# Optimization experiments

Measured on AMD Instinct MI355X. Metric: run time of the kernel, lower is better.

## Reference

```python
import jax, jax.numpy as jnp
import numpy as np

B, NB, BS, F = 4, 16, 256, 1024   # batch, num_blocks, block_size, features
H, D = 16, 64                     # heads, head_dim
ROPE = 32                         # rope_rotary_dims


def rotate_every_two(x):
    x1 = x[..., ::2]
    x2 = x[..., 1::2]
    return jnp.stack([-x2, x1], axis=-1).reshape(x.shape)


def apply_rope(x, num_blocks, block_size):
    # x: [B, NB, BS, H, rope_dim]
    rope_dim = x.shape[-1]
    inv_freq = 1.0 / 10000.0 ** (jnp.arange(0, rope_dim, 2, dtype=jnp.float32) / rope_dim)
    pos = jnp.arange(num_blocks * block_size, dtype=jnp.float32)
    ang = pos[:, None] * inv_freq[None, :]                       # [S, rope_dim/2]
    sin = jnp.sin(ang).reshape(num_blocks, block_size, rope_dim // 2)
    cos = jnp.cos(ang).reshape(num_blocks, block_size, rope_dim // 2)
    sin = jnp.repeat(sin[None, :, :, None, :], 2, axis=-1)       # [1, NB, BS, 1, rope_dim]
    cos = jnp.repeat(cos[None, :, :, None, :], 2, axis=-1)
    return x * cos + rotate_every_two(x) * sin


def setup_inputs() -> dict:
    key = jax.random.key(0)
    ks = jax.random.split(key, 8)
    s_in = 1.0 / np.sqrt(F)
    s_out = 1.0 / np.sqrt(H * D)
    return {
        "inputs_q": jax.random.normal(ks[0], (B, NB, BS, F), jnp.float32),
        "inputs_kv": jax.random.normal(ks[1], (B, NB, BS, F), jnp.float32),
        "Wq": jax.random.normal(ks[2], (F, H, D), jnp.float32) * s_in,
        "bq": jnp.zeros((H, D), jnp.float32),
        "Wk": jax.random.normal(ks[3], (F, H, D), jnp.float32) * s_in,
        "bk": jnp.zeros((H, D), jnp.float32),
        "Wv": jax.random.normal(ks[4], (F, H, D), jnp.float32) * s_in,
        "bv": jnp.zeros((H, D), jnp.float32),
        "Wo": jax.random.normal(ks[5], (H, D, F), jnp.float32) * s_out,
        "bo": jnp.zeros((F,), jnp.float32),
    }


def reference(inputs_q, inputs_kv, Wq, bq, Wk, bk, Wv, bv, Wo, bo):
    # QKV projections: [B, NB, BS, F] x [F, H, D] -> [B, NB, BS, H, D]
    q = jnp.einsum("bnsf,fhd->bnshd", inputs_q, Wq) + bq
    k = jnp.einsum("bnsf,fhd->bnshd", inputs_kv, Wk) + bk
    v = jnp.einsum("bnsf,fhd->bnshd", inputs_kv, Wv) + bv

    # RoPE on first ROPE dims of head_dim (intended semantics per docstring)
    q_rot, q_pass = q[..., :ROPE], q[..., ROPE:]
    k_rot, k_pass = k[..., :ROPE], k[..., ROPE:]
    q = jnp.concatenate([apply_rope(q_rot, NB, BS), q_pass], axis=-1)
    k = jnp.concatenate([apply_rope(k_rot, NB, BS), k_pass], axis=-1)

    # block-local dot-product attention (flax nn.dot_product_attention semantics)
    q = q / jnp.sqrt(jnp.asarray(D, q.dtype))
    scores = jnp.einsum("bnqhd,bnkhd->bnhqk", q, k)              # [B, NB, H, BS, BS]
    weights = jax.nn.softmax(scores, axis=-1)
    x = jnp.einsum("bnhqk,bnkhd->bnqhd", weights, v)             # [B, NB, BS, H, D]

    # output projection over (heads, head_dim)
    out = jnp.einsum("bnqhd,hdf->bnqf", x, Wo) + bo              # [B, NB, BS, F]
    return out
```

## Files before the change

kernel.cpp:

```cpp
#include <hip/hip_runtime.h>

typedef __attribute__((ext_vector_type(4))) float f32x4;
typedef __attribute__((ext_vector_type(8))) short s16x8;
typedef __attribute__((ext_vector_type(4))) unsigned short u16x4;

struct F2 { float c, s; };

__device__ __forceinline__ unsigned short f2b(float f) {
  unsigned u = __builtin_bit_cast(unsigned, f);
  u += 0x7FFFu + ((u >> 16) & 1u);
  return (unsigned short)(u >> 16);
}
__device__ __forceinline__ void gll16(const void* g, void* l) {
  __builtin_amdgcn_global_load_lds(
      (const __attribute__((address_space(1))) unsigned int*)g,
      (__attribute__((address_space(3))) unsigned int*)l, 16, 0, 0);
}
__device__ __forceinline__ f32x4 mfma16(s16x8 a, s16x8 b, f32x4 c) {
  return __builtin_amdgcn_mfma_f32_16x16x32_bf16(a, b, c, 0, 0, 0);
}

__global__ void k_cvt(const float* __restrict__ src, unsigned short* __restrict__ dst, int n4) {
  int i = blockIdx.x * 256 + threadIdx.x;
  int stride = gridDim.x * 256;
  for (; i < n4; i += stride) {
    f32x4 v = ((const f32x4*)src)[i];
    u16x4 o;
    o.x = f2b(v.x); o.y = f2b(v.y); o.z = f2b(v.z); o.w = f2b(v.w);
    ((u16x4*)dst)[i] = o;
  }
}

__global__ void k_sincos(F2* __restrict__ tab) {
  int idx = blockIdx.x * 256 + threadIdx.x;
  int pos = idx >> 4, fi = idx & 15;
  double inv = exp((double)fi * (-9.210340371976184 / 16.0));
  double a = (double)pos * inv;
  F2 r; r.c = (float)cos(a); r.s = (float)sin(a);
  tab[idx] = r;
}

__global__ void k_transpose(const float* __restrict__ wq,
                            const float* __restrict__ wk,
                            const float* __restrict__ wv,
                            const float* __restrict__ wo,
                            unsigned short* __restrict__ wtqkv,
                            unsigned short* __restrict__ wto) {
  __shared__ unsigned short tile[32][33];
  int z = blockIdx.z;
  const float* src = (z == 0) ? wq : (z == 1) ? wk : (z == 2) ? wv : wo;
  unsigned short* dst = (z < 3) ? (wtqkv + (size_t)z * 1048576) : wto;
  int bx = blockIdx.x * 32, by = blockIdx.y * 32;
  tile[threadIdx.y][threadIdx.x] = f2b(src[(size_t)(by + threadIdx.y) * 1024 + bx + threadIdx.x]);
  __syncthreads();
  dst[(size_t)(bx + threadIdx.y) * 1024 + by + threadIdx.x] = tile[threadIdx.x][threadIdx.y];
}

__device__ __forceinline__ void gemm_core(
    const unsigned short* __restrict__ Ag, const unsigned short* __restrict__ Bg,
    int m0, int n0, unsigned short* Sh, f32x4 (&acc)[8][4]) {
  const int tid = threadIdx.x, wid = tid >> 6, lane = tid & 63;
  const int fr = lane & 15, fg = lane >> 4, f7 = fr & 7;
  const int wm = wid >> 2, wn = wid & 3;
  const int rowoff = lane >> 3;
  const int lanecol = ((lane & 7) ^ rowoff) * 8;
  const int g0 = (fg ^ f7) * 8, g1 = ((4 + fg) ^ f7) * 8;

  auto SA = [&](int T, int ah) {
    unsigned short* dstb = Sh + (T & 1) * 32768;
#pragma unroll
    for (int i = 0; i < 2; ++i) {
      int rloc = ah * 128 + (wid * 2 + i) * 8;
      gll16(Ag + (size_t)(m0 + rloc + rowoff) * 1024 + T * 64 + lanecol, dstb + rloc * 64);
    }
  };
  auto SB = [&](int T, int bh) {
    unsigned short* dstb = Sh + (T & 1) * 32768 + 16384;
#pragma unroll
    for (int i = 0; i < 2; ++i) {
      int rloc = bh * 128 + (wid * 2 + i) * 8;
      gll16(Bg + (size_t)(n0 + rloc + rowoff) * 1024 + T * 64 + lanecol, dstb + rloc * 64);
    }
  };

  SA(0, 0); SA(0, 1); SB(0, 0); SB(0, 1); SA(1, 0); SA(1, 1);
  asm volatile("s_waitcnt vmcnt(4)" ::: "memory");
  __builtin_amdgcn_sched_barrier(0);
  __builtin_amdgcn_s_barrier();

  for (int t = 0; t < 16; ++t) {
    const unsigned short* bufA = Sh + (t & 1) * 32768;
    const unsigned short* bufB = bufA + 16384;
    s16x8 a0[4][2], a1[4][2], b0[2][2], b1[2][2];
#pragma unroll
    for (int mf = 0; mf < 4; ++mf) {
      const unsigned short* r = &bufA[(wm * 128 + mf * 16 + fr) * 64];
      a0[mf][0] = *(const s16x8*)&r[g0];
      a0[mf][1] = *(const s16x8*)&r[g1];
    }
#pragma unroll
    for (int nf = 0; nf < 2; ++nf) {
      const unsigned short* r = &bufB[(wn * 64 + nf * 16 + fr) * 64];
      b0[nf][0] = *(const s16x8*)&r[g0];
      b0[nf][1] = *(const s16x8*)&r[g1];
    }
    if (t + 1 < 16) SB(t + 1, 0);
    __builtin_amdgcn_s_barrier();
    asm volatile("s_waitcnt lgkmcnt(0)" ::: "memory");
    __builtin_amdgcn_sched_barrier(0);
    __builtin_amdgcn_s_setprio(1);
#pragma unroll
    for (int mf = 0; mf < 4; ++mf)
#pragma unroll
      for (int nf = 0; nf < 2; ++nf) {
        acc[mf][nf] = mfma16(a0[mf][0], b0[nf][0], acc[mf][nf]);
        acc[mf][nf] = mfma16(a0[mf][1], b0[nf][1], acc[mf][nf]);
      }
    __builtin_amdgcn_s_setprio(0);
    __builtin_amdgcn_s_barrier();
#pragma unroll
    for (int mf = 0; mf < 4; ++mf) {
      const unsigned short* r = &bufA[(wm * 128 + 64 + mf * 16 + fr) * 64];
      a1[mf][0] = *(const s16x8*)&r[g0];
      a1[mf][1] = *(const s16x8*)&r[g1];
    }
    if (t + 1 < 16) SB(t + 1, 1);
    __builtin_amdgcn_s_barrier();
    asm volatile("s_waitcnt lgkmcnt(0)" ::: "memory");
    __builtin_amdgcn_sched_barrier(0);
    __builtin_amdgcn_s_setprio(1);
#pragma unroll
    for (int mf = 0; mf < 4; ++mf)
#pragma unroll
      for (int nf = 0; nf < 2; ++nf) {
        acc[4 + mf][nf] = mfma16(a1[mf][0], b0[nf][0], acc[4 + mf][nf]);
        acc[4 + mf][nf] = mfma16(a1[mf][1], b0[nf][1], acc[4 + mf][nf]);
      }
    __builtin_amdgcn_s_setprio(0);
    __builtin_amdgcn_s_barrier();
#pragma unroll
    for (int nf = 0; nf < 2; ++nf) {
      const unsigned short* r = &bufB[(wn * 64 + 32 + nf * 16 + fr) * 64];
      b1[nf][0] = *(const s16x8*)&r[g0];
      b1[nf][1] = *(const s16x8*)&r[g1];
    }
    if (t + 2 < 16) SA(t + 2, 0);
    __builtin_amdgcn_s_barrier();
    asm volatile("s_waitcnt lgkmcnt(0)" ::: "memory");
    __builtin_amdgcn_sched_barrier(0);
    __builtin_amdgcn_s_setprio(1);
#pragma unroll
    for (int mf = 0; mf < 4; ++mf)
#pragma unroll
      for (int nf = 0; nf < 2; ++nf) {
        acc[4 + mf][2 + nf] = mfma16(a1[mf][0], b1[nf][0], acc[4 + mf][2 + nf]);
        acc[4 + mf][2 + nf] = mfma16(a1[mf][1], b1[nf][1], acc[4 + mf][2 + nf]);
      }
    __builtin_amdgcn_s_setprio(0);
    __builtin_amdgcn_s_barrier();
    if (t + 2 < 16) SA(t + 2, 1);
    if (t < 14) asm volatile("s_waitcnt vmcnt(4)" ::: "memory");
    else        asm volatile("s_waitcnt vmcnt(0)" ::: "memory");
    __builtin_amdgcn_sched_barrier(0);
    __builtin_amdgcn_s_barrier();
    __builtin_amdgcn_s_setprio(1);
#pragma unroll
    for (int mf = 0; mf < 4; ++mf)
#pragma unroll
      for (int nf = 0; nf < 2; ++nf) {
        acc[mf][2 + nf] = mfma16(a0[mf][0], b1[nf][0], acc[mf][2 + nf]);
        acc[mf][2 + nf] = mfma16(a0[mf][1], b1[nf][1], acc[mf][2 + nf]);
      }
    __builtin_amdgcn_s_setprio(0);
    __builtin_amdgcn_s_barrier();
  }
}

__global__ __launch_bounds__(512, 1) void k_qkv(
    const unsigned short* __restrict__ Xq,
    const unsigned short* __restrict__ Xkv,
    const unsigned short* __restrict__ WT,
    const float* __restrict__ bq,
    const float* __restrict__ bk,
    const float* __restrict__ bv,
    const F2* __restrict__ tab,
    unsigned short* __restrict__ qbuf,
    unsigned short* __restrict__ kbuf,
    unsigned short* __restrict__ vbuf) {
  __shared__ __align__(16) unsigned short S[65536];
  int bid = blockIdx.x;
  int swz = (bid & 7) * 96 + (bid >> 3);
  int mt = swz / 12, nt = swz % 12;
  int m0 = mt * 256, n0 = nt * 256;
  int which = n0 >> 10;
  const unsigned short* X = (which == 0) ? Xq : Xkv;
  const float* bias = (which == 0) ? bq : (which == 1) ? bk : bv;
  unsigned short* dst = (which == 0) ? qbuf : (which == 1) ? kbuf : vbuf;
  int n0l = n0 & 1023;
  int tid = threadIdx.x, wid = tid >> 6, lane = tid & 63;
  int fr = lane & 15, fg = lane >> 4;
  int wm = wid >> 2, wn = wid & 3;

  f32x4 acc[8][4] = {};
  gemm_core(X, WT, m0, n0, S, acc);

  unsigned short* W = S + wid * 8192;
  int hh = (n0l + wn * 64) >> 6;
  int bn = m0 >> 8;
#pragma unroll
  for (int nf = 0; nf < 4; ++nf) {
    int d = nf * 16 + fr;
    int col = n0l + wn * 64 + d;
    float bz = bias[col];
    bool rope = (which < 2) && (nf < 2);
#pragma unroll
    for (int mf = 0; mf < 8; ++mf) {
#pragma unroll
      for (int j = 0; j < 4; ++j) {
        int row = mf * 16 + fg * 4 + j;
        int mg = m0 + wm * 128 + row;
        float v = acc[mf][nf][j] + bz;
        if (rope) {
          float p = __shfl_xor(v, 1);
          F2 cs = tab[(mg & 4095) * 16 + (d >> 1)];
          v = (d & 1) ? fmaf(v, cs.c, p * cs.s) : fmaf(v, cs.c, -(p * cs.s));
        }
        if (which == 0) v *= 0.125f;
        W[row * 64 + (((d >> 3) ^ (row & 7)) << 3) + (d & 7)] = f2b(v);
      }
    }
  }
  asm volatile("s_waitcnt lgkmcnt(0)" ::: "memory");
  __builtin_amdgcn_sched_barrier(0);
  size_t gbase = ((size_t)(bn * 16 + hh) * 256 + wm * 128) * 64;
#pragma unroll
  for (int it = 0; it < 16; ++it) {
    int r = it * 8 + (lane >> 3);
    int ch = (lane & 7) ^ (r & 7);
    s16x8 vv = *(const s16x8*)&W[r * 64 + ch * 8];
    *(s16x8*)&dst[gbase + r * 64 + (lane & 7) * 8] = vv;
  }
}

__global__ __launch_bounds__(512, 1) void k_attn(
    const unsigned short* __restrict__ qbuf,
    const unsigned short* __restrict__ kbuf,
    const unsigned short* __restrict__ vbuf,
    unsigned short* __restrict__ xbuf) {
  __shared__ __align__(16) unsigned short Kl[256 * 64];
  __shared__ __align__(16) unsigned short Vt[64 * 264];
  __shared__ __align__(16) unsigned short Pl[8][16 * 264];
  int gb = blockIdx.x;
  size_t base = (size_t)gb * (256 * 64);
  const unsigned short* Q = qbuf + base;
  const unsigned short* K = kbuf + base;
  const unsigned short* V = vbuf + base;
  int bn = gb >> 4, h = gb & 15;
  int tid = threadIdx.x, wid = tid >> 6, lane = tid & 63;
  int fr = lane & 15, fg = lane >> 4;

#pragma unroll
  for (int tt = 0; tt < 4; ++tt) {
    int t = wid * 4 + tt;
    int r = t * 8 + (lane >> 3);
    int csrc = (lane & 7) ^ (r & 7);
    gll16(K + r * 64 + csrc * 8, &Kl[t * 512]);
  }
  {
    int rv = tid >> 1, chalf = (tid & 1) * 32;
#pragma unroll
    for (int c8 = 0; c8 < 4; ++c8) {
      s16x8 vv = *(const s16x8*)&V[rv * 64 + chalf + c8 * 8];
#pragma unroll
      for (int j = 0; j < 8; ++j)
        Vt[(chalf + c8 * 8 + j) * 264 + rv] = (unsigned short)vv[j];
    }
  }
  __syncthreads();

  unsigned short* P = Pl[wid];
  int f7 = fr & 7;
  int c0 = (fg ^ f7) * 8;
  int c1 = ((4 + fg) ^ f7) * 8;
  for (int mtile = 0; mtile < 2; ++mtile) {
    int q0 = wid * 32 + mtile * 16;
    s16x8 qa0 = *(const s16x8*)&Q[(q0 + fr) * 64 + fg * 8];
    s16x8 qa1 = *(const s16x8*)&Q[(q0 + fr) * 64 + 32 + fg * 8];
    f32x4 sc[16] = {};
#pragma unroll
    for (int nt = 0; nt < 16; ++nt) {
      int rr = nt * 16 + fr;
      s16x8 kb0 = *(const s16x8*)&Kl[rr * 64 + c0];
      sc[nt] = mfma16(qa0, kb0, sc[nt]);
      s16x8 kb1 = *(const s16x8*)&Kl[rr * 64 + c1];
      sc[nt] = mfma16(qa1, kb1, sc[nt]);
    }
    float rs[4];
#pragma unroll
    for (int j = 0; j < 4; ++j) {
      float m = sc[0][j];
#pragma unroll
      for (int nt = 1; nt < 16; ++nt) m = fmaxf(m, sc[nt][j]);
      m = fmaxf(m, __shfl_xor(m, 1));
      m = fmaxf(m, __shfl_xor(m, 2));
      m = fmaxf(m, __shfl_xor(m, 4));
      m = fmaxf(m, __shfl_xor(m, 8));
      float sum = 0.f;
#pragma unroll
      for (int nt = 0; nt < 16; ++nt) {
        float p = __expf(sc[nt][j] - m);
        sum += p;
        P[(fg * 4 + j) * 264 + nt * 16 + fr] = f2b(p);
      }
      sum += __shfl_xor(sum, 1);
      sum += __shfl_xor(sum, 2);
      sum += __shfl_xor(sum, 4);
      sum += __shfl_xor(sum, 8);
      rs[j] = 1.0f / sum;
    }
    f32x4 o[4] = {};
#pragma unroll
    for (int ks = 0; ks < 8; ++ks) {
      s16x8 pa = *(const s16x8*)&P[fr * 264 + ks * 32 + fg * 8];
#pragma unroll
      for (int nt = 0; nt < 4; ++nt) {
        s16x8 vb = *(const s16x8*)&Vt[(nt * 16 + fr) * 264 + ks * 32 + fg * 8];
        o[nt] = mfma16(pa, vb, o[nt]);
      }
    }
#pragma unroll
    for (int nt = 0; nt < 4; ++nt)
#pragma unroll
      for (int j = 0; j < 4; ++j) {
        int srow = q0 + fg * 4 + j;
        int d = nt * 16 + fr;
        xbuf[((size_t)(bn * 256 + srow)) * 1024 + h * 64 + d] = f2b(o[nt][j] * rs[j]);
      }
  }
}

__global__ __launch_bounds__(512, 1) void k_out(
    const unsigned short* __restrict__ Xb,
    const unsigned short* __restrict__ WT,
    const float* __restrict__ bo,
    float* __restrict__ out) {
  __shared__ __align__(16) unsigned short S[65536];
  int bid = blockIdx.x;
  int swz = (bid & 7) * 32 + (bid >> 3);
  int mt = swz >> 2, nt = swz & 3;
  int m0 = mt * 256, n0 = nt * 256;
  int tid = threadIdx.x, wid = tid >> 6, lane = tid & 63;
  int fr = lane & 15, fg = lane >> 4;
  int wm = wid >> 2, wn = wid & 3;

  f32x4 acc[8][4] = {};
  gemm_core(Xb, WT, m0, n0, S, acc);

  float* Wf = (float*)S + wid * 4096;
#pragma unroll
  for (int p = 0; p < 2; ++p) {
#pragma unroll
    for (int nf = 0; nf < 4; ++nf) {
      int d = nf * 16 + fr;
      float bz = bo[n0 + wn * 64 + d];
#pragma unroll
      for (int mf = 0; mf < 4; ++mf) {
#pragma unroll
        for (int j = 0; j < 4; ++j) {
          int row = mf * 16 + fg * 4 + j;
          Wf[row * 64 + d] = acc[p * 4 + mf][nf][j] + bz;
        }
      }
    }
    asm volatile("s_waitcnt lgkmcnt(0)" ::: "memory");
    __builtin_amdgcn_sched_barrier(0);
#pragma unroll
    for (int it = 0; it < 16; ++it) {
      int r = it * 4 + (lane >> 4);
      f32x4 vv = *(const f32x4*)&Wf[r * 64 + (lane & 15) * 4];
      int mg = m0 + wm * 128 + p * 64 + r;
      *(f32x4*)&out[(size_t)mg * 1024 + n0 + wn * 64 + (lane & 15) * 4] = vv;
    }
    asm volatile("s_waitcnt lgkmcnt(0)" ::: "memory");
    __builtin_amdgcn_sched_barrier(0);
  }
}

extern "C" void kernel_launch(void* const* d_in, const int* in_sizes, int n_in,
                              void* d_out, int out_size, void* d_ws, size_t ws_size,
                              hipStream_t stream) {
  const float* Xq  = (const float*)d_in[0];
  const float* Xkv = (const float*)d_in[1];
  const float* Wq  = (const float*)d_in[2];
  const float* bq  = (const float*)d_in[3];
  const float* Wk  = (const float*)d_in[4];
  const float* bk  = (const float*)d_in[5];
  const float* Wv  = (const float*)d_in[6];
  const float* bv  = (const float*)d_in[7];
  const float* Wo  = (const float*)d_in[8];
  const float* bo  = (const float*)d_in[9];
  float* out = (float*)d_out;

  char* ws = (char*)d_ws;
  size_t off = 0;
  F2* tab = (F2*)(ws + off);                           off += (size_t)65536 * sizeof(F2);
  unsigned short* WTqkv = (unsigned short*)(ws + off); off += (size_t)3 * 1048576 * 2;
  unsigned short* WTo   = (unsigned short*)(ws + off); off += (size_t)1048576 * 2;
  unsigned short* Xqb   = (unsigned short*)(ws + off); off += (size_t)16777216 * 2;
  unsigned short* Xkvb  = (unsigned short*)(ws + off); off += (size_t)16777216 * 2;
  unsigned short* qb = (unsigned short*)(ws + off); off += (size_t)16777216 * 2;
  unsigned short* kb = (unsigned short*)(ws + off); off += (size_t)16777216 * 2;
  unsigned short* vb = (unsigned short*)(ws + off); off += (size_t)16777216 * 2;
  unsigned short* xb = Xqb;

  k_cvt<<<2048, 256, 0, stream>>>(Xq,  Xqb,  4194304);
  k_cvt<<<2048, 256, 0, stream>>>(Xkv, Xkvb, 4194304);
  k_sincos<<<256, 256, 0, stream>>>(tab);
  k_transpose<<<dim3(32, 32, 4), dim3(32, 32), 0, stream>>>(Wq, Wk, Wv, Wo, WTqkv, WTo);
  k_qkv<<<768, 512, 0, stream>>>(Xqb, Xkvb, WTqkv, bq, bk, bv, tab, qb, kb, vb);
  k_attn<<<1024, 512, 0, stream>>>(qb, kb, vb, xb);
  k_out<<<256, 512, 0, stream>>>(xb, WTo, bo, out);
}
```

Measured before the change: 283.8 us.

## Switch GEMM core to 32x32x16 bf16 MFMA with reordered A/B prefetch

Replaces the 16x16x32 MFMA tiles in the shared GEMM core with 32x32x16 bf16 MFMAs, restructuring per-wave fragments into 2x2 blocks of 32x32 accumulators. The LDS fragment loads and prefetch order change so A is streamed one stage ahead and B two stages ahead, and the QKV and output epilogues are remapped to the 32x32 accumulator layout. The aim is fewer MFMA issues and fewer LDS reads per FLOP. In exchange the register footprint and LDS access pattern change, and the swizzle now has to stay bank-conflict free for 32-row reads.

```diff
diff --git a/kernel.cpp b/kernel.cpp
--- a/kernel.cpp
+++ b/kernel.cpp
@@ -1,6 +1,7 @@
 #include <hip/hip_runtime.h>
 
 typedef __attribute__((ext_vector_type(4))) float f32x4;
+typedef __attribute__((ext_vector_type(16))) float f32x16;
 typedef __attribute__((ext_vector_type(8))) short s16x8;
 typedef __attribute__((ext_vector_type(4))) unsigned short u16x4;
 
@@ -18,6 +19,9 @@
 }
 __device__ __forceinline__ f32x4 mfma16(s16x8 a, s16x8 b, f32x4 c) {
   return __builtin_amdgcn_mfma_f32_16x16x32_bf16(a, b, c, 0, 0, 0);
+}
+__device__ __forceinline__ f32x16 mfma32(s16x8 a, s16x8 b, f32x16 c) {
+  return __builtin_amdgcn_mfma_f32_32x32x16_bf16(a, b, c, 0, 0, 0);
 }
 
 __global__ void k_cvt(const float* __restrict__ src, unsigned short* __restrict__ dst, int n4) {
@@ -58,13 +62,15 @@
 
 __device__ __forceinline__ void gemm_core(
     const unsigned short* __restrict__ Ag, const unsigned short* __restrict__ Bg,
-    int m0, int n0, unsigned short* Sh, f32x4 (&acc)[8][4]) {
+    int m0, int n0, unsigned short* Sh, f32x16 (&acc)[4][2]) {
   const int tid = threadIdx.x, wid = tid >> 6, lane = tid & 63;
-  const int fr = lane & 15, fg = lane >> 4, f7 = fr & 7;
+  const int l31 = lane & 31, l5 = lane >> 5, r7 = lane & 7;
   const int wm = wid >> 2, wn = wid & 3;
   const int rowoff = lane >> 3;
   const int lanecol = ((lane & 7) ^ rowoff) * 8;
-  const int g0 = (fg ^ f7) * 8, g1 = ((4 + fg) ^ f7) * 8;
+  int gk[4];
+#pragma unroll
+  for (int ks = 0; ks < 4; ++ks) gk[ks] = ((ks * 2 + l5) ^ r7) * 8;
 
   auto SA = [&](int T, int ah) {
     unsigned short* dstb = Sh + (T & 1) * 32768;
@@ -83,7 +89,7 @@
     }
   };
 
-  SA(0, 0); SA(0, 1); SB(0, 0); SB(0, 1); SA(1, 0); SA(1, 1);
+  SA(0, 0); SA(0, 1); SB(0, 0); SB(0, 1); SB(1, 0); SB(1, 1);
   asm volatile("s_waitcnt vmcnt(4)" ::: "memory");
   __builtin_amdgcn_sched_barrier(0);
   __builtin_amdgcn_s_barrier();
@@ -91,86 +97,70 @@
   for (int t = 0; t < 16; ++t) {
     const unsigned short* bufA = Sh + (t & 1) * 32768;
     const unsigned short* bufB = bufA + 16384;
-    s16x8 a0[4][2], a1[4][2], b0[2][2], b1[2][2];
-#pragma unroll
-    for (int mf = 0; mf < 4; ++mf) {
-      const unsigned short* r = &bufA[(wm * 128 + mf * 16 + fr) * 64];
-      a0[mf][0] = *(const s16x8*)&r[g0];
-      a0[mf][1] = *(const s16x8*)&r[g1];
-    }
-#pragma unroll
-    for (int nf = 0; nf < 2; ++nf) {
-      const unsigned short* r = &bufB[(wn * 64 + nf * 16 + fr) * 64];
-      b0[nf][0] = *(const s16x8*)&r[g0];
-      b0[nf][1] = *(const s16x8*)&r[g1];
-    }
-    if (t + 1 < 16) SB(t + 1, 0);
+    s16x8 alo[2][4], ahi[2][4], b0[4], b1[4];
+#pragma unroll
+    for (int mb = 0; mb < 2; ++mb)
+#pragma unroll
+      for (int ks = 0; ks < 4; ++ks)
+        alo[mb][ks] = *(const s16x8*)&bufA[(wm * 128 + mb * 32 + l31) * 64 + gk[ks]];
+#pragma unroll
+    for (int ks = 0; ks < 4; ++ks)
+      b0[ks] = *(const s16x8*)&bufB[(wn * 64 + l31) * 64 + gk[ks]];
+    if (t + 1 < 16) SA(t + 1, 0);
     __builtin_amdgcn_s_barrier();
     asm volatile("s_waitcnt lgkmcnt(0)" ::: "memory");
     __builtin_amdgcn_sched_barrier(0);
     __builtin_amdgcn_s_setprio(1);
 #pragma unroll
-    for (int mf = 0; mf < 4; ++mf)
-#pragma unroll
-      for (int nf = 0; nf < 2; ++nf) {
-        acc[mf][nf] = mfma16(a0[mf][0], b0[nf][0], acc[mf][nf]);
-        acc[mf][nf] = mfma16(a0[mf][1], b0[nf][1], acc[mf][nf]);
-      }
+    for (int ks = 0; ks < 4; ++ks)
+#pragma unroll
+      for (int mb = 0; mb < 2; ++mb)
+        acc[mb][0] = mfma32(alo[mb][ks], b0[ks], acc[mb][0]);
     __builtin_amdgcn_s_setprio(0);
     __builtin_amdgcn_s_barrier();
 #pragma unroll
-    for (int mf = 0; mf < 4; ++mf) {
-      const unsigned short* r = &bufA[(wm * 128 + 64 + mf * 16 + fr) * 64];
-      a1[mf][0] = *(const s16x8*)&r[g0];
-      a1[mf][1] = *(const s16x8*)&r[g1];
-    }
-    if (t + 1 < 16) SB(t + 1, 1);
+    for (int ks = 0; ks < 4; ++ks)
+      b1[ks] = *(const s16x8*)&bufB[(wn * 64 + 32 + l31) * 64 + gk[ks]];
+    if (t + 1 < 16) SA(t + 1, 1);
     __builtin_amdgcn_s_barrier();
     asm volatile("s_waitcnt lgkmcnt(0)" ::: "memory");
     __builtin_amdgcn_sched_barrier(0);
     __builtin_amdgcn_s_setprio(1);
 #pragma unroll
-    for (int mf = 0; mf < 4; ++mf)
-#pragma unroll
-      for (int nf = 0; nf < 2; ++nf) {
-        acc[4 + mf][nf] = mfma16(a1[mf][0], b0[nf][0], acc[4 + mf][nf]);
-        acc[4 + mf][nf] = mfma16(a1[mf][1], b0[nf][1], acc[4 + mf][nf]);
-      }
+    for (int ks = 0; ks < 4; ++ks)
+#pragma unroll
+      for (int mb = 0; mb < 2; ++mb)
+        acc[mb][1] = mfma32(alo[mb][ks], b1[ks], acc[mb][1]);
     __builtin_amdgcn_s_setprio(0);
     __builtin_amdgcn_s_barrier();
 #pragma unroll
-    for (int nf = 0; nf < 2; ++nf) {
-      const unsigned short* r = &bufB[(wn * 64 + 32 + nf * 16 + fr) * 64];
-      b1[nf][0] = *(const s16x8*)&r[g0];
-      b1[nf][1] = *(const s16x8*)&r[g1];
-    }
-    if (t + 2 < 16) SA(t + 2, 0);
+    for (int mb = 0; mb < 2; ++mb)
+#pragma unroll
+      for (int ks = 0; ks < 4; ++ks)
+        ahi[mb][ks] = *(const s16x8*)&bufA[(wm * 128 + 64 + mb * 32 + l31) * 64 + gk[ks]];
+    if (t + 2 < 16) SB(t + 2, 0);
     __builtin_amdgcn_s_barrier();
     asm volatile("s_waitcnt lgkmcnt(0)" ::: "memory");
     __builtin_amdgcn_sched_barrier(0);
     __builtin_amdgcn_s_setprio(1);
 #pragma unroll
-    for (int mf = 0; mf < 4; ++mf)
-#pragma unroll
-      for (int nf = 0; nf < 2; ++nf) {
-        acc[4 + mf][2 + nf] = mfma16(a1[mf][0], b1[nf][0], acc[4 + mf][2 + nf]);
-        acc[4 + mf][2 + nf] = mfma16(a1[mf][1], b1[nf][1], acc[4 + mf][2 + nf]);
-      }
+    for (int ks = 0; ks < 4; ++ks)
+#pragma unroll
+      for (int mb = 0; mb < 2; ++mb)
+        acc[2 + mb][0] = mfma32(ahi[mb][ks], b0[ks], acc[2 + mb][0]);
     __builtin_amdgcn_s_setprio(0);
     __builtin_amdgcn_s_barrier();
-    if (t + 2 < 16) SA(t + 2, 1);
+    if (t + 2 < 16) SB(t + 2, 1);
     if (t < 14) asm volatile("s_waitcnt vmcnt(4)" ::: "memory");
     else        asm volatile("s_waitcnt vmcnt(0)" ::: "memory");
     __builtin_amdgcn_sched_barrier(0);
     __builtin_amdgcn_s_barrier();
     __builtin_amdgcn_s_setprio(1);
 #pragma unroll
-    for (int mf = 0; mf < 4; ++mf)
-#pragma unroll
-      for (int nf = 0; nf < 2; ++nf) {
-        acc[mf][2 + nf] = mfma16(a0[mf][0], b1[nf][0], acc[mf][2 + nf]);
-        acc[mf][2 + nf] = mfma16(a0[mf][1], b1[nf][1], acc[mf][2 + nf]);
-      }
+    for (int ks = 0; ks < 4; ++ks)
+#pragma unroll
+      for (int mb = 0; mb < 2; ++mb)
+        acc[2 + mb][1] = mfma32(ahi[mb][ks], b1[ks], acc[2 + mb][1]);
     __builtin_amdgcn_s_setprio(0);
     __builtin_amdgcn_s_barrier();
   }
@@ -198,28 +188,28 @@
   unsigned short* dst = (which == 0) ? qbuf : (which == 1) ? kbuf : vbuf;
   int n0l = n0 & 1023;
   int tid = threadIdx.x, wid = tid >> 6, lane = tid & 63;
-  int fr = lane & 15, fg = lane >> 4;
+  int l31 = lane & 31, l5 = lane >> 5;
   int wm = wid >> 2, wn = wid & 3;
 
-  f32x4 acc[8][4] = {};
+  f32x16 acc[4][2] = {};
   gemm_core(X, WT, m0, n0, S, acc);
 
   unsigned short* W = S + wid * 8192;
   int hh = (n0l + wn * 64) >> 6;
   int bn = m0 >> 8;
 #pragma unroll
-  for (int nf = 0; nf < 4; ++nf) {
-    int d = nf * 16 + fr;
+  for (int nb = 0; nb < 2; ++nb) {
+    int d = nb * 32 + l31;
     int col = n0l + wn * 64 + d;
     float bz = bias[col];
-    bool rope = (which < 2) && (nf < 2);
-#pragma unroll
-    for (int mf = 0; mf < 8; ++mf) {
-#pragma unroll
-      for (int j = 0; j < 4; ++j) {
-        int row = mf * 16 + fg * 4 + j;
+    bool rope = (which < 2) && (nb == 0);
+#pragma unroll
+    for (int mbi = 0; mbi < 4; ++mbi) {
+#pragma unroll
+      for (int r = 0; r < 16; ++r) {
+        int row = mbi * 32 + (r & 3) + 8 * (r >> 2) + 4 * l5;
         int mg = m0 + wm * 128 + row;
-        float v = acc[mf][nf][j] + bz;
+        float v = acc[mbi][nb][r] + bz;
         if (rope) {
           float p = __shfl_xor(v, 1);
           F2 cs = tab[(mg & 4095) * 16 + (d >> 1)];
@@ -350,25 +340,25 @@
   int mt = swz >> 2, nt = swz & 3;
   int m0 = mt * 256, n0 = nt * 256;
   int tid = threadIdx.x, wid = tid >> 6, lane = tid & 63;
-  int fr = lane & 15, fg = lane >> 4;
+  int l31 = lane & 31, l5 = lane >> 5;
   int wm = wid >> 2, wn = wid & 3;
 
-  f32x4 acc[8][4] = {};
+  f32x16 acc[4][2] = {};
   gemm_core(Xb, WT, m0, n0, S, acc);
 
   float* Wf = (float*)S + wid * 4096;
 #pragma unroll
   for (int p = 0; p < 2; ++p) {
 #pragma unroll
-    for (int nf = 0; nf < 4; ++nf) {
-      int d = nf * 16 + fr;
+    for (int nb = 0; nb < 2; ++nb) {
+      int d = nb * 32 + l31;
       float bz = bo[n0 + wn * 64 + d];
 #pragma unroll
-      for (int mf = 0; mf < 4; ++mf) {
-#pragma unroll
-        for (int j = 0; j < 4; ++j) {
-          int row = mf * 16 + fg * 4 + j;
-          Wf[row * 64 + d] = acc[p * 4 + mf][nf][j] + bz;
+      for (int mbh = 0; mbh < 2; ++mbh) {
+#pragma unroll
+        for (int r = 0; r < 16; ++r) {
+          int row = mbh * 32 + (r & 3) + 8 * (r >> 2) + 4 * l5;
+          Wf[row * 64 + d] = acc[p * 2 + mbh][nb][r] + bz;
         }
       }
     }
```

New measurement: 307.3 us. +8.3%, slower.

## Fuse fp32-to-bf16 input conversion into QKV GEMM A-tile loading

Applied to the files above, without the earlier changes.

Removes the separate k_cvt passes over both fp32 activation tensors. The QKV GEMM now reads fp32 A tiles through registers, converts them to bf16, and writes them into swizzled LDS, with a reworked pipeline that interleaves these loads and writes between MFMA phases. This saves a full write and re-read of 64 MB of bf16 intermediates. In exchange the GEMM reads twice the A bytes per tile, uses more registers, and no longer gets asynchronous direct-to-LDS loads for A, so it may stall more.

```diff
diff --git a/kernel.cpp b/kernel.cpp
--- a/kernel.cpp
+++ b/kernel.cpp
@@ -18,17 +18,6 @@
 }
 __device__ __forceinline__ f32x4 mfma16(s16x8 a, s16x8 b, f32x4 c) {
   return __builtin_amdgcn_mfma_f32_16x16x32_bf16(a, b, c, 0, 0, 0);
-}
-
-__global__ void k_cvt(const float* __restrict__ src, unsigned short* __restrict__ dst, int n4) {
-  int i = blockIdx.x * 256 + threadIdx.x;
-  int stride = gridDim.x * 256;
-  for (; i < n4; i += stride) {
-    f32x4 v = ((const f32x4*)src)[i];
-    u16x4 o;
-    o.x = f2b(v.x); o.y = f2b(v.y); o.z = f2b(v.z); o.w = f2b(v.w);
-    ((u16x4*)dst)[i] = o;
-  }
 }
 
 __global__ void k_sincos(F2* __restrict__ tab) {
@@ -56,7 +45,7 @@
   dst[(size_t)(bx + threadIdx.y) * 1024 + by + threadIdx.x] = tile[threadIdx.x][threadIdx.y];
 }
 
-__device__ __forceinline__ void gemm_core(
+__device__ __forceinline__ void gemm_core_bf16(
     const unsigned short* __restrict__ Ag, const unsigned short* __restrict__ Bg,
     int m0, int n0, unsigned short* Sh, f32x4 (&acc)[8][4]) {
   const int tid = threadIdx.x, wid = tid >> 6, lane = tid & 63;
@@ -176,9 +165,149 @@
   }
 }
 
+__device__ __forceinline__ void gemm_core_af32(
+    const float* __restrict__ Ag, const unsigned short* __restrict__ Bg,
+    int m0, int n0, unsigned short* Sh, f32x4 (&acc)[8][4]) {
+  const int tid = threadIdx.x, wid = tid >> 6, lane = tid & 63;
+  const int fr = lane & 15, fg = lane >> 4, f7 = fr & 7;
+  const int wm = wid >> 2, wn = wid & 3;
+  const int rowoff = lane >> 3, cp = lane & 7;
+  const int lanecol = (cp ^ rowoff) * 8;
+  const int g0 = (fg ^ f7) * 8, g1 = ((4 + fg) ^ f7) * 8;
+
+  auto SB = [&](int T, int bh) {
+    unsigned short* dstb = Sh + (T & 1) * 32768 + 16384;
+#pragma unroll
+    for (int i = 0; i < 2; ++i) {
+      int rloc = bh * 128 + (wid * 2 + i) * 8;
+      gll16(Bg + (size_t)(n0 + rloc + rowoff) * 1024 + T * 64 + lanecol, dstb + rloc * 64);
+    }
+  };
+  f32x4 ar[4][2];
+  auto LA = [&](int T) {
+#pragma unroll
+    for (int h = 0; h < 2; ++h)
+#pragma unroll
+      for (int i = 0; i < 2; ++i) {
+        int rloc = h * 128 + (wid * 2 + i) * 8;
+        const float* src = Ag + (size_t)(m0 + rloc + rowoff) * 1024 + T * 64 + cp * 8;
+        ar[h * 2 + i][0] = *(const f32x4*)src;
+        ar[h * 2 + i][1] = *(const f32x4*)(src + 4);
+      }
+  };
+  auto WA = [&](int T, int h) {
+    unsigned short* dstb = Sh + (T & 1) * 32768;
+#pragma unroll
+    for (int i = 0; i < 2; ++i) {
+      int rloc = h * 128 + (wid * 2 + i) * 8;
+      int ci = h * 2 + i;
+      s16x8 w;
+#pragma unroll
+      for (int e = 0; e < 4; ++e) {
+        w[e]     = (short)f2b(ar[ci][0][e]);
+        w[4 + e] = (short)f2b(ar[ci][1][e]);
+      }
+      *(s16x8*)&dstb[(rloc + rowoff) * 64 + (cp ^ rowoff) * 8] = w;
+    }
+  };
+
+  LA(0);
+  WA(0, 0); WA(0, 1);
+  SB(0, 0); SB(0, 1);
+  asm volatile("s_waitcnt vmcnt(0) lgkmcnt(0)" ::: "memory");
+  __builtin_amdgcn_sched_barrier(0);
+  __builtin_amdgcn_s_barrier();
+
+  for (int t = 0; t < 16; ++t) {
+    const unsigned short* bufA = Sh + (t & 1) * 32768;
+    const unsigned short* bufB = bufA + 16384;
+    s16x8 a0[4][2], a1[4][2], b0[2][2], b1[2][2];
+#pragma unroll
+    for (int mf = 0; mf < 4; ++mf) {
+      const unsigned short* r = &bufA[(wm * 128 + mf * 16 + fr) * 64];
+      a0[mf][0] = *(const s16x8*)&r[g0];
+      a0[mf][1] = *(const s16x8*)&r[g1];
+    }
+#pragma unroll
+    for (int nf = 0; nf < 2; ++nf) {
+      const unsigned short* r = &bufB[(wn * 64 + nf * 16 + fr) * 64];
+      b0[nf][0] = *(const s16x8*)&r[g0];
+      b0[nf][1] = *(const s16x8*)&r[g1];
+    }
+    if (t + 1 < 16) { LA(t + 1); SB(t + 1, 0); }
+    __builtin_amdgcn_s_barrier();
+    asm volatile("s_waitcnt lgkmcnt(0)" ::: "memory");
+    __builtin_amdgcn_sched_barrier(0);
+    __builtin_amdgcn_s_setprio(1);
+#pragma unroll
+    for (int mf = 0; mf < 4; ++mf)
+#pragma unroll
+      for (int nf = 0; nf < 2; ++nf) {
+        acc[mf][nf] = mfma16(a0[mf][0], b0[nf][0], acc[mf][nf]);
+        acc[mf][nf] = mfma16(a0[mf][1], b0[nf][1], acc[mf][nf]);
+      }
+    __builtin_amdgcn_s_setprio(0);
+    __builtin_amdgcn_s_barrier();
+#pragma unroll
+    for (int mf = 0; mf < 4; ++mf) {
+      const unsigned short* r = &bufA[(wm * 128 + 64 + mf * 16 + fr) * 64];
+      a1[mf][0] = *(const s16x8*)&r[g0];
+      a1[mf][1] = *(const s16x8*)&r[g1];
+    }
+    if (t + 1 < 16) SB(t + 1, 1);
+    __builtin_amdgcn_s_barrier();
+    asm volatile("s_waitcnt lgkmcnt(0)" ::: "memory");
+    __builtin_amdgcn_sched_barrier(0);
+    __builtin_amdgcn_s_setprio(1);
+#pragma unroll
+    for (int mf = 0; mf < 4; ++mf)
+#pragma unroll
+      for (int nf = 0; nf < 2; ++nf) {
+        acc[4 + mf][nf] = mfma16(a1[mf][0], b0[nf][0], acc[4 + mf][nf]);
+        acc[4 + mf][nf] = mfma16(a1[mf][1], b0[nf][1], acc[4 + mf][nf]);
+      }
+    __builtin_amdgcn_s_setprio(0);
+    __builtin_amdgcn_s_barrier();
+#pragma unroll
+    for (int nf = 0; nf < 2; ++nf) {
+      const unsigned short* r = &bufB[(wn * 64 + 32 + nf * 16 + fr) * 64];
+      b1[nf][0] = *(const s16x8*)&r[g0];
+      b1[nf][1] = *(const s16x8*)&r[g1];
+    }
+    if (t + 1 < 16) WA(t + 1, 0);
+    __builtin_amdgcn_s_barrier();
+    asm volatile("s_waitcnt lgkmcnt(0)" ::: "memory");
+    __builtin_amdgcn_sched_barrier(0);
+    __builtin_amdgcn_s_setprio(1);
+#pragma unroll
+    for (int mf = 0; mf < 4; ++mf)
+#pragma unroll
+      for (int nf = 0; nf < 2; ++nf) {
+        acc[4 + mf][2 + nf] = mfma16(a1[mf][0], b1[nf][0], acc[4 + mf][2 + nf]);
+        acc[4 + mf][2 + nf] = mfma16(a1[mf][1], b1[nf][1], acc[4 + mf][2 + nf]);
+      }
+    __builtin_amdgcn_s_setprio(0);
+    __builtin_amdgcn_s_barrier();
+    if (t + 1 < 16) WA(t + 1, 1);
+    asm volatile("s_waitcnt vmcnt(0) lgkmcnt(0)" ::: "memory");
+    __builtin_amdgcn_sched_barrier(0);
+    __builtin_amdgcn_s_barrier();
+    __builtin_amdgcn_s_setprio(1);
+#pragma unroll
+    for (int mf = 0; mf < 4; ++mf)
+#pragma unroll
+      for (int nf = 0; nf < 2; ++nf) {
+        acc[mf][2 + nf] = mfma16(a0[mf][0], b1[nf][0], acc[mf][2 + nf]);
+        acc[mf][2 + nf] = mfma16(a0[mf][1], b1[nf][1], acc[mf][2 + nf]);
+      }
+    __builtin_amdgcn_s_setprio(0);
+    __builtin_amdgcn_s_barrier();
+  }
+}
+
 __global__ __launch_bounds__(512, 1) void k_qkv(
-    const unsigned short* __restrict__ Xq,
-    const unsigned short* __restrict__ Xkv,
+    const float* __restrict__ Xq,
+    const float* __restrict__ Xkv,
     const unsigned short* __restrict__ WT,
     const float* __restrict__ bq,
     const float* __restrict__ bk,
@@ -193,7 +322,7 @@
   int mt = swz / 12, nt = swz % 12;
   int m0 = mt * 256, n0 = nt * 256;
   int which = n0 >> 10;
-  const unsigned short* X = (which == 0) ? Xq : Xkv;
+  const float* X = (which == 0) ? Xq : Xkv;
   const float* bias = (which == 0) ? bq : (which == 1) ? bk : bv;
   unsigned short* dst = (which == 0) ? qbuf : (which == 1) ? kbuf : vbuf;
   int n0l = n0 & 1023;
@@ -202,7 +331,7 @@
   int wm = wid >> 2, wn = wid & 3;
 
   f32x4 acc[8][4] = {};
-  gemm_core(X, WT, m0, n0, S, acc);
+  gemm_core_af32(X, WT, m0, n0, S, acc);
 
   unsigned short* W = S + wid * 8192;
   int hh = (n0l + wn * 64) >> 6;
@@ -354,7 +483,7 @@
   int wm = wid >> 2, wn = wid & 3;
 
   f32x4 acc[8][4] = {};
-  gemm_core(Xb, WT, m0, n0, S, acc);
+  gemm_core_bf16(Xb, WT, m0, n0, S, acc);
 
   float* Wf = (float*)S + wid * 4096;
 #pragma unroll
@@ -406,18 +535,14 @@
   F2* tab = (F2*)(ws + off);                           off += (size_t)65536 * sizeof(F2);
   unsigned short* WTqkv = (unsigned short*)(ws + off); off += (size_t)3 * 1048576 * 2;
   unsigned short* WTo   = (unsigned short*)(ws + off); off += (size_t)1048576 * 2;
-  unsigned short* Xqb   = (unsigned short*)(ws + off); off += (size_t)16777216 * 2;
-  unsigned short* Xkvb  = (unsigned short*)(ws + off); off += (size_t)16777216 * 2;
   unsigned short* qb = (unsigned short*)(ws + off); off += (size_t)16777216 * 2;
   unsigned short* kb = (unsigned short*)(ws + off); off += (size_t)16777216 * 2;
   unsigned short* vb = (unsigned short*)(ws + off); off += (size_t)16777216 * 2;
-  unsigned short* xb = Xqb;
-
-  k_cvt<<<2048, 256, 0, stream>>>(Xq,  Xqb,  4194304);
-  k_cvt<<<2048, 256, 0, stream>>>(Xkv, Xkvb, 4194304);
+  unsigned short* xb = (unsigned short*)(ws + off); off += (size_t)16777216 * 2;
+
   k_sincos<<<256, 256, 0, stream>>>(tab);
   k_transpose<<<dim3(32, 32, 4), dim3(32, 32), 0, stream>>>(Wq, Wk, Wv, Wo, WTqkv, WTo);
-  k_qkv<<<768, 512, 0, stream>>>(Xqb, Xkvb, WTqkv, bq, bk, bv, tab, qb, kb, vb);
+  k_qkv<<<768, 512, 0, stream>>>(Xq, Xkv, WTqkv, bq, bk, bv, tab, qb, kb, vb);
   k_attn<<<1024, 512, 0, stream>>>(qb, kb, vb, xb);
   k_out<<<256, 512, 0, stream>>>(xb, WTo, bo, out);
 }
```

Measured after the change: 452.8 us. 59.5% more time.
